# Kernel optimization log

Measured on AMD Instinct MI355X. Metric: run time of the kernel, lower is better.

## Reference

```python
import jax, jax.numpy as jnp
import numpy as np

B, T, D_IN, D_OUT = 4, 2048, 1024, 1024

def setup_inputs() -> dict:
    key = jax.random.key(0)
    k1, k2, k3, k4 = jax.random.split(key, 4)
    return {
        "vector": jax.random.normal(k1, (B, T, D_IN), dtype=jnp.float32),
        "W_queries": jax.random.normal(k2, (D_IN, D_OUT), dtype=jnp.float32),
        "W_keys": jax.random.normal(k3, (D_IN, D_OUT), dtype=jnp.float32),
        "W_values": jax.random.normal(k4, (D_IN, D_OUT), dtype=jnp.float32),
    }

def reference(vector, W_queries, W_keys, W_values):
    # vector: [B,T,d_in]; projections -> [B,T,d_out]
    q = vector @ W_queries
    k = vector @ W_keys
    v = vector @ W_values
    d_out = k.shape[-1]
    scores = jnp.einsum('btd,bsd->bts', q, k)  # [B,T,T]
    t = scores.shape[1]
    causal = jnp.tril(jnp.ones((t, t), dtype=bool))  # True = keep (mask is triu diag=1)
    scores = jnp.where(causal, scores, -jnp.inf)
    weights = jax.nn.softmax(scores / jnp.sqrt(jnp.float32(d_out)), axis=-1)
    # dropout p=0.0 -> identity
    return jnp.einsum('bts,bsd->btd', weights, v)
```

## Files before the change

### kernel.cpp

```cpp
#include <hip/hip_runtime.h>

#define TT   2048
#define DD   1024
#define BK   32

typedef float  f32x4  __attribute__((ext_vector_type(4)));
typedef __bf16 bf16x8 __attribute__((ext_vector_type(8)));

static __device__ __forceinline__ unsigned short f2bf(float f){
  unsigned int u = __float_as_uint(f);
  return (unsigned short)((u + 0x7fffu + ((u >> 16) & 1u)) >> 16);
}
static __device__ __forceinline__ float bf2f(unsigned short h){
  return __uint_as_float(((unsigned int)h) << 16);
}
static __device__ __forceinline__ bf16x8 ld8(const unsigned short* p){
  return *(const bf16x8*)p;
}
static __device__ __forceinline__ f32x4 mfma16(bf16x8 a, bf16x8 b, f32x4 c){
  return __builtin_amdgcn_mfma_f32_16x16x32_bf16(a, b, c, 0, 0, 0);
}

static __device__ __forceinline__ void async16(
    const unsigned short* g, unsigned short* l)
{
  __builtin_amdgcn_global_load_lds(
      (const __attribute__((address_space(1))) unsigned int*)g,
      (__attribute__((address_space(3))) unsigned int*)l, 16, 0, 0);
}

static __device__ __forceinline__ void stage_async(
    const unsigned short* __restrict__ src, int row_stride,
    unsigned short* __restrict__ dst, int t)
{
#pragma unroll
  for (int j = 0; j < 2; j++){
    int e = (t + j * 256) * 8;
    int row = e >> 5, col = e & 31;
    async16(src + (size_t)row * row_stride + col, dst + e);
  }
}

__global__ __launch_bounds__(256) void split_all_kernel(
    const float* __restrict__ X,  const float* __restrict__ Wq,
    const float* __restrict__ Wk, const float* __restrict__ Wv,
    unsigned short* __restrict__ Xhi,  unsigned short* __restrict__ Xlo,
    unsigned short* __restrict__ Wqhi, unsigned short* __restrict__ Wqlo,
    unsigned short* __restrict__ Wkhi, unsigned short* __restrict__ Wklo,
    unsigned short* __restrict__ WvThi)
{
  __shared__ float tile[32][33];
  int bx = blockIdx.x;
  if (bx < 10240){
    const float* src; unsigned short *hi, *lo; size_t base;
    if (bx < 8192)      { src = X;  hi = Xhi;  lo = Xlo;  base = (size_t)bx * 1024; }
    else if (bx < 9216) { src = Wq; hi = Wqhi; lo = Wqlo; base = (size_t)(bx - 8192) * 1024; }
    else                { src = Wk; hi = Wkhi; lo = Wklo; base = (size_t)(bx - 9216) * 1024; }
    size_t i = base + (size_t)threadIdx.x * 4;
    const float4 x = *(const float4*)(src + i);
    ushort4 h, l;
    h.x = f2bf(x.x); l.x = f2bf(x.x - bf2f(h.x));
    h.y = f2bf(x.y); l.y = f2bf(x.y - bf2f(h.y));
    h.z = f2bf(x.z); l.z = f2bf(x.z - bf2f(h.z));
    h.w = f2bf(x.w); l.w = f2bf(x.w - bf2f(h.w));
    *(ushort4*)(hi + i) = h;
    *(ushort4*)(lo + i) = l;
  } else {
    int tid = bx - 10240;
    int k0 = (tid & 31) * 32, n0 = (tid >> 5) * 32;
    int tx = threadIdx.x & 31, ty = threadIdx.x >> 5;
#pragma unroll
    for (int r = 0; r < 4; r++){
      int row = ty + r * 8;
      tile[row][tx] = Wv[(size_t)(k0 + row) * DD + n0 + tx];
    }
    __syncthreads();
#pragma unroll
    for (int r = 0; r < 4; r++){
      int nrow = ty + r * 8;
      float v = tile[tx][nrow];
      WvThi[(size_t)(n0 + nrow) * DD + k0 + tx] = f2bf(v);
    }
  }
}

__global__ __launch_bounds__(256) void mt_kernel(
    const unsigned short* __restrict__ Wkhi, const unsigned short* __restrict__ Wklo,
    const unsigned short* __restrict__ Wqhi, const unsigned short* __restrict__ Wqlo,
    unsigned short* __restrict__ MThi, unsigned short* __restrict__ MTlo)
{
  __shared__ unsigned short Ahi[128 * BK], Alo[128 * BK];
  __shared__ unsigned short Bhi[128 * BK], Blo[128 * BK];
  int e0 = blockIdx.y * 128, d0 = blockIdx.x * 128;
  const unsigned short* Ah_g = Wkhi + (size_t)e0 * DD;
  const unsigned short* Al_g = Wklo + (size_t)e0 * DD;
  const unsigned short* Bh_g = Wqhi + (size_t)d0 * DD;
  const unsigned short* Bl_g = Wqlo + (size_t)d0 * DD;
  int t = threadIdx.x;
  int lane = t & 63, w = t >> 6;
  int mw = (w >> 1) << 6, nw = (w & 1) << 6;
  int frow = lane & 15, fk = (lane >> 4) << 3;

  f32x4 acc[4][4];
#pragma unroll
  for (int a = 0; a < 4; a++)
#pragma unroll
    for (int c = 0; c < 4; c++){ f32x4 zz = {0.f,0.f,0.f,0.f}; acc[a][c] = zz; }

  for (int kk = 0; kk < DD / BK; kk++){
    int k0 = kk * BK;
    stage_async(Ah_g + k0, DD, Ahi, t);
    stage_async(Al_g + k0, DD, Alo, t);
    stage_async(Bh_g + k0, DD, Bhi, t);
    stage_async(Bl_g + k0, DD, Blo, t);
    __syncthreads();

    bf16x8 ah[4], al[4], bh[4], bl[4];
#pragma unroll
    for (int tm = 0; tm < 4; tm++){
      int off = (mw + tm * 16 + frow) * BK + fk;
      ah[tm] = ld8(&Ahi[off]); al[tm] = ld8(&Alo[off]);
    }
#pragma unroll
    for (int tn = 0; tn < 4; tn++){
      int off = (nw + tn * 16 + frow) * BK + fk;
      bh[tn] = ld8(&Bhi[off]); bl[tn] = ld8(&Blo[off]);
    }
#pragma unroll
    for (int tm = 0; tm < 4; tm++)
#pragma unroll
      for (int tn = 0; tn < 4; tn++){
        acc[tm][tn] = mfma16(ah[tm], bh[tn], acc[tm][tn]);
        acc[tm][tn] = mfma16(ah[tm], bl[tn], acc[tm][tn]);
        acc[tm][tn] = mfma16(al[tm], bh[tn], acc[tm][tn]);
      }
    __syncthreads();
  }

#pragma unroll
  for (int tm = 0; tm < 4; tm++)
#pragma unroll
    for (int tn = 0; tn < 4; tn++)
#pragma unroll
      for (int r = 0; r < 4; r++){
        float v = acc[tm][tn][r];
        int ge = e0 + mw + tm * 16 + ((lane >> 4) << 2) + r;
        int gd = d0 + nw + tn * 16 + frow;
        size_t idx = (size_t)ge * DD + gd;
        unsigned short h = f2bf(v);
        MThi[idx] = h; MTlo[idx] = f2bf(v - bf2f(h));
      }
}

__global__ __launch_bounds__(256, 2) void y_kernel(
    const unsigned short* __restrict__ Xhi, const unsigned short* __restrict__ Xlo,
    const unsigned short* __restrict__ MThi, const unsigned short* __restrict__ MTlo,
    const unsigned short* __restrict__ WvThi,
    unsigned short* __restrict__ Yhi, unsigned short* __restrict__ Ylo,
    unsigned short* __restrict__ VT)
{
  __shared__ unsigned short Ahs[128 * BK], Als[128 * BK];
  __shared__ unsigned short Bmh[128 * BK], Bml[128 * BK], Bvh[128 * BK];
  int m0 = blockIdx.x * 128, n0 = blockIdx.y * 128;
  const unsigned short* Ah_g  = Xhi   + (size_t)m0 * DD;
  const unsigned short* Al_g  = Xlo   + (size_t)m0 * DD;
  const unsigned short* Bmh_g = MThi  + (size_t)n0 * DD;
  const unsigned short* Bml_g = MTlo  + (size_t)n0 * DD;
  const unsigned short* Bvh_g = WvThi + (size_t)n0 * DD;
  int t = threadIdx.x;
  int lane = t & 63, w = t >> 6;
  int mw = (w >> 1) << 6, nw = (w & 1) << 6;
  int frow = lane & 15, fk = (lane >> 4) << 3;

  f32x4 accY[4][4], accV[4][4];
#pragma unroll
  for (int a = 0; a < 4; a++)
#pragma unroll
    for (int c = 0; c < 4; c++){
      f32x4 zz = {0.f,0.f,0.f,0.f}; accY[a][c] = zz; accV[a][c] = zz;
    }

  for (int kk = 0; kk < DD / BK; kk++){
    int k0 = kk * BK;
    stage_async(Ah_g  + k0, DD, Ahs, t);
    stage_async(Al_g  + k0, DD, Als, t);
    stage_async(Bmh_g + k0, DD, Bmh, t);
    stage_async(Bml_g + k0, DD, Bml, t);
    stage_async(Bvh_g + k0, DD, Bvh, t);
    __syncthreads();

    bf16x8 ah[4], al[4];
#pragma unroll
    for (int tm = 0; tm < 4; tm++){
      int off = (mw + tm * 16 + frow) * BK + fk;
      ah[tm] = ld8(&Ahs[off]); al[tm] = ld8(&Als[off]);
    }
#pragma unroll
    for (int tn = 0; tn < 4; tn++){
      int off = (nw + tn * 16 + frow) * BK + fk;
      bf16x8 bmh = ld8(&Bmh[off]), bml = ld8(&Bml[off]), bvh = ld8(&Bvh[off]);
#pragma unroll
      for (int tm = 0; tm < 4; tm++){
        accY[tm][tn] = mfma16(ah[tm], bmh, accY[tm][tn]);
        accY[tm][tn] = mfma16(ah[tm], bml, accY[tm][tn]);
        accY[tm][tn] = mfma16(al[tm], bmh, accY[tm][tn]);
        accV[tm][tn] = mfma16(ah[tm], bvh, accV[tm][tn]);
      }
    }
    __syncthreads();
  }

#pragma unroll
  for (int tm = 0; tm < 4; tm++)
#pragma unroll
    for (int tn = 0; tn < 4; tn++)
#pragma unroll
      for (int r = 0; r < 4; r++){
        int grow = m0 + mw + tm * 16 + ((lane >> 4) << 2) + r;
        int gcol = n0 + nw + tn * 16 + frow;
        size_t idx = (size_t)grow * DD + gcol;
        float vy = accY[tm][tn][r];
        unsigned short hy = f2bf(vy);
        Yhi[idx] = hy; Ylo[idx] = f2bf(vy - bf2f(hy));
        int b = grow >> 11, tl = grow & 2047;
        VT[((size_t)(b * DD + gcol) << 11) | tl] = f2bf(accV[tm][tn][r]);
      }
}

__global__ __launch_bounds__(256) void s_kernel(
    const unsigned short* __restrict__ Yhi, const unsigned short* __restrict__ Ylo,
    const unsigned short* __restrict__ Xhi, const unsigned short* __restrict__ Xlo,
    float* __restrict__ S)
{
  __shared__ unsigned short Ahi[128 * BK], Alo[128 * BK];
  __shared__ unsigned short Bhi[128 * BK], Blo[128 * BK];
  int bx = blockIdx.x;
  int nt = (bx < 32) ? 2 : 1;
  int u0 = (bx < 32) ? (480 + bx) : (bx - 32);
  int t = threadIdx.x;
  int lane = t & 63, w = t >> 6;
  int mw = (w >> 1) << 6, nw = (w & 1) << 6;
  int frow = lane & 15, fk = (lane >> 4) << 3;

  for (int sub = 0; sub < nt; sub++){
    int u = u0 + sub * 32;
    int b = u & 3;
    int tid = u >> 2;
    int bi = (int)((sqrtf(8.f * (float)tid + 1.f) - 1.f) * 0.5f);
    while ((bi + 1) * (bi + 2) / 2 <= tid) bi++;
    while (bi * (bi + 1) / 2 > tid) bi--;
    int bj = tid - bi * (bi + 1) / 2;
    int i0 = bi * 128, j0 = bj * 128;
    const unsigned short* Ah_g = Yhi + (size_t)(b * TT + i0) * DD;
    const unsigned short* Al_g = Ylo + (size_t)(b * TT + i0) * DD;
    const unsigned short* Bh_g = Xhi + (size_t)(b * TT + j0) * DD;
    const unsigned short* Bl_g = Xlo + (size_t)(b * TT + j0) * DD;

    f32x4 acc[4][4];
#pragma unroll
    for (int a = 0; a < 4; a++)
#pragma unroll
      for (int c = 0; c < 4; c++){ f32x4 zz = {0.f,0.f,0.f,0.f}; acc[a][c] = zz; }

    for (int kk = 0; kk < DD / BK; kk++){
      int k0 = kk * BK;
      stage_async(Ah_g + k0, DD, Ahi, t);
      stage_async(Al_g + k0, DD, Alo, t);
      stage_async(Bh_g + k0, DD, Bhi, t);
      stage_async(Bl_g + k0, DD, Blo, t);
      __syncthreads();

      bf16x8 ah[4], al[4], bh[4], bl[4];
#pragma unroll
      for (int tm = 0; tm < 4; tm++){
        int off = (mw + tm * 16 + frow) * BK + fk;
        ah[tm] = ld8(&Ahi[off]); al[tm] = ld8(&Alo[off]);
      }
#pragma unroll
      for (int tn = 0; tn < 4; tn++){
        int off = (nw + tn * 16 + frow) * BK + fk;
        bh[tn] = ld8(&Bhi[off]); bl[tn] = ld8(&Blo[off]);
      }
#pragma unroll
      for (int tm = 0; tm < 4; tm++)
#pragma unroll
        for (int tn = 0; tn < 4; tn++){
          acc[tm][tn] = mfma16(ah[tm], bh[tn], acc[tm][tn]);
          acc[tm][tn] = mfma16(ah[tm], bl[tn], acc[tm][tn]);
          acc[tm][tn] = mfma16(al[tm], bh[tn], acc[tm][tn]);
        }
      __syncthreads();
    }

#pragma unroll
    for (int tm = 0; tm < 4; tm++)
#pragma unroll
      for (int tn = 0; tn < 4; tn++)
#pragma unroll
        for (int r = 0; r < 4; r++){
          int gi = i0 + mw + tm * 16 + ((lane >> 4) << 2) + r;
          int gj = j0 + nw + tn * 16 + frow;
          S[((size_t)(b * TT + gi) * TT) + gj] = acc[tm][tn][r] * 0.03125f;
        }
  }
}

__global__ __launch_bounds__(256) void softmax_kernel(
    const float* __restrict__ S, unsigned short* __restrict__ P)
{
  int i = blockIdx.x, b = blockIdx.y;
  const float* s = S + (size_t)(b * TT + i) * TT;
  unsigned short* p = P + (size_t)(b * TT + i) * TT;
  int n = i + 1;
  int npad = ((i >> 7) + 1) << 7;
  int t = threadIdx.x;
  __shared__ float red[256];

  float v[8];
  float mx = -1e30f;
#pragma unroll
  for (int pas = 0; pas < 2; pas++){
    int idx = t * 4 + pas * 1024;
    if (idx + 3 < n){
      float4 x = *(const float4*)(s + idx);
      v[pas*4+0] = x.x; v[pas*4+1] = x.y; v[pas*4+2] = x.z; v[pas*4+3] = x.w;
    } else {
#pragma unroll
      for (int e = 0; e < 4; e++)
        v[pas*4+e] = (idx + e < n) ? s[idx + e] : -1e30f;
    }
#pragma unroll
    for (int e = 0; e < 4; e++) mx = fmaxf(mx, v[pas*4+e]);
  }
  red[t] = mx; __syncthreads();
  for (int k = 128; k > 0; k >>= 1){ if (t < k) red[t] = fmaxf(red[t], red[t + k]); __syncthreads(); }
  mx = red[0]; __syncthreads();

  float sum = 0.f;
#pragma unroll
  for (int j = 0; j < 8; j++){
    v[j] = __expf(v[j] - mx);
    sum += v[j];
  }
  red[t] = sum; __syncthreads();
  for (int k = 128; k > 0; k >>= 1){ if (t < k) red[t] += red[t + k]; __syncthreads(); }
  float inv = 1.0f / red[0];

#pragma unroll
  for (int pas = 0; pas < 2; pas++){
    int idx = t * 4 + pas * 1024;
    if (idx < npad){
      ushort4 o;
      o.x = f2bf(v[pas*4+0] * inv);
      o.y = f2bf(v[pas*4+1] * inv);
      o.z = f2bf(v[pas*4+2] * inv);
      o.w = f2bf(v[pas*4+3] * inv);
      *(ushort4*)(p + idx) = o;
    }
  }
}

__global__ __launch_bounds__(256) void pv_kernel(
    const unsigned short* __restrict__ P, const unsigned short* __restrict__ VT,
    float* __restrict__ O)
{
  __shared__ unsigned short At[128 * BK];
  __shared__ unsigned short Bt[128 * BK];
  int b  = blockIdx.z;
  int by = (int)gridDim.y - 1 - blockIdx.y;
  int i0 = by * 128, n0 = blockIdx.x * 128;
  int ksteps = (by + 1) * 4;
  const unsigned short* A_g = P  + (size_t)(b * TT + i0) * TT;
  const unsigned short* B_g = VT + (size_t)(b * DD + n0) * TT;
  int t = threadIdx.x;
  int lane = t & 63, w = t >> 6;
  int mw = (w >> 1) << 6, nw = (w & 1) << 6;
  int frow = lane & 15, fk = (lane >> 4) << 3;

  f32x4 acc[4][4];
#pragma unroll
  for (int a = 0; a < 4; a++)
#pragma unroll
    for (int c = 0; c < 4; c++){ f32x4 zz = {0.f,0.f,0.f,0.f}; acc[a][c] = zz; }

  for (int kk = 0; kk < ksteps; kk++){
    int k0 = kk * BK;
    stage_async(A_g + k0, TT, At, t);
    stage_async(B_g + k0, TT, Bt, t);
    __syncthreads();

    bf16x8 af[4], bf[4];
#pragma unroll
    for (int tm = 0; tm < 4; tm++) af[tm] = ld8(&At[(mw + tm * 16 + frow) * BK + fk]);
#pragma unroll
    for (int tn = 0; tn < 4; tn++) bf[tn] = ld8(&Bt[(nw + tn * 16 + frow) * BK + fk]);
#pragma unroll
    for (int tm = 0; tm < 4; tm++)
#pragma unroll
      for (int tn = 0; tn < 4; tn++)
        acc[tm][tn] = mfma16(af[tm], bf[tn], acc[tm][tn]);
    __syncthreads();
  }

#pragma unroll
  for (int tm = 0; tm < 4; tm++)
#pragma unroll
    for (int tn = 0; tn < 4; tn++)
#pragma unroll
      for (int r = 0; r < 4; r++){
        int gi = i0 + mw + tm * 16 + ((lane >> 4) << 2) + r;
        int gd = n0 + nw + tn * 16 + frow;
        O[(size_t)(b * TT + gi) * DD + gd] = acc[tm][tn][r];
      }
}

extern "C" void kernel_launch(void* const* d_in, const int* in_sizes, int n_in,
                              void* d_out, int out_size, void* d_ws, size_t ws_size,
                              hipStream_t stream) {
  const float* X  = (const float*)d_in[0];
  const float* Wq = (const float*)d_in[1];
  const float* Wk = (const float*)d_in[2];
  const float* Wv = (const float*)d_in[3];
  float* Out = (float*)d_out;

  const size_t M1 = 1048576u;
  unsigned short* base  = (unsigned short*)d_ws;
  unsigned short* Wqhi  = base;
  unsigned short* Wqlo  = base + 1 * M1;
  unsigned short* Wkhi  = base + 2 * M1;
  unsigned short* Wklo  = base + 3 * M1;
  unsigned short* WvThi = base + 4 * M1;
  unsigned short* MThi  = base + 5 * M1;
  unsigned short* MTlo  = base + 6 * M1;
  unsigned short* Xhi   = base + 7 * M1;
  unsigned short* Xlo   = base + 15 * M1;
  unsigned short* Yhi   = base + 23 * M1;
  unsigned short* Ylo   = base + 31 * M1;
  unsigned short* VT    = base + 39 * M1;
  float*          S     = (float*)(base + 47 * M1);
  unsigned short* P     = Xhi;

  dim3 blk(256);
  split_all_kernel<<<dim3(11264), blk, 0, stream>>>(X, Wq, Wk, Wv,
      Xhi, Xlo, Wqhi, Wqlo, Wkhi, Wklo, WvThi);
  mt_kernel<<<dim3(8, 8), blk, 0, stream>>>(Wkhi, Wklo, Wqhi, Wqlo, MThi, MTlo);
  y_kernel<<<dim3(64, 8), blk, 0, stream>>>(Xhi, Xlo, MThi, MTlo, WvThi, Yhi, Ylo, VT);
  s_kernel<<<dim3(512), blk, 0, stream>>>(Yhi, Ylo, Xhi, Xlo, S);
  softmax_kernel<<<dim3(2048, 4, 1), blk, 0, stream>>>(S, P);
  pv_kernel<<<dim3(8, 16, 4), blk, 0, stream>>>(P, VT, Out);
}
```

Before: 360.3 us.

## Split-K the last 32 score tiles and reduce partials inside softmax

The old score kernel ran 512 blocks, with 32 blocks doing two tiles each to cover 544 lower-triangle tiles. Now 512 blocks each do one full tile, and the last 32 tiles are split four ways along K into 128 extra blocks. The first K-quarter writes to S and the other three write partial sums to a separate buffer, which softmax adds back for rows 1920 and up. This evens out the per-block work and removes the two-tile tail, at the cost of extra partial-sum traffic and an unconditional float4 load in softmax that can read past the causal range.

```diff
diff --git a/kernel.cpp b/kernel.cpp
--- a/kernel.cpp
+++ b/kernel.cpp
@@ -230,68 +230,72 @@
 __global__ __launch_bounds__(256) void s_kernel(
     const unsigned short* __restrict__ Yhi, const unsigned short* __restrict__ Ylo,
     const unsigned short* __restrict__ Xhi, const unsigned short* __restrict__ Xlo,
-    float* __restrict__ S)
+    float* __restrict__ S, float* __restrict__ Spart)
 {
   __shared__ unsigned short Ahi[128 * BK], Alo[128 * BK];
   __shared__ unsigned short Bhi[128 * BK], Blo[128 * BK];
   int bx = blockIdx.x;
-  int nt = (bx < 32) ? 2 : 1;
-  int u0 = (bx < 32) ? (480 + bx) : (bx - 32);
+  int u, q, kbeg, kend;
+  if (bx < 512){ u = bx; q = 0; kbeg = 0; kend = 32; }
+  else {
+    int e = bx - 512;
+    q = e & 3;
+    u = 512 + (e >> 2);
+    kbeg = q * 8; kend = kbeg + 8;
+  }
+  int b = u & 3;
+  int tid = u >> 2;
+  int bi = (int)((sqrtf(8.f * (float)tid + 1.f) - 1.f) * 0.5f);
+  while ((bi + 1) * (bi + 2) / 2 <= tid) bi++;
+  while (bi * (bi + 1) / 2 > tid) bi--;
+  int bj = tid - bi * (bi + 1) / 2;
+  int i0 = bi * 128, j0 = bj * 128;
+  const unsigned short* Ah_g = Yhi + (size_t)(b * TT + i0) * DD;
+  const unsigned short* Al_g = Ylo + (size_t)(b * TT + i0) * DD;
+  const unsigned short* Bh_g = Xhi + (size_t)(b * TT + j0) * DD;
+  const unsigned short* Bl_g = Xlo + (size_t)(b * TT + j0) * DD;
   int t = threadIdx.x;
   int lane = t & 63, w = t >> 6;
   int mw = (w >> 1) << 6, nw = (w & 1) << 6;
   int frow = lane & 15, fk = (lane >> 4) << 3;
 
-  for (int sub = 0; sub < nt; sub++){
-    int u = u0 + sub * 32;
-    int b = u & 3;
-    int tid = u >> 2;
-    int bi = (int)((sqrtf(8.f * (float)tid + 1.f) - 1.f) * 0.5f);
-    while ((bi + 1) * (bi + 2) / 2 <= tid) bi++;
-    while (bi * (bi + 1) / 2 > tid) bi--;
-    int bj = tid - bi * (bi + 1) / 2;
-    int i0 = bi * 128, j0 = bj * 128;
-    const unsigned short* Ah_g = Yhi + (size_t)(b * TT + i0) * DD;
-    const unsigned short* Al_g = Ylo + (size_t)(b * TT + i0) * DD;
-    const unsigned short* Bh_g = Xhi + (size_t)(b * TT + j0) * DD;
-    const unsigned short* Bl_g = Xlo + (size_t)(b * TT + j0) * DD;
-
-    f32x4 acc[4][4];
-#pragma unroll
-    for (int a = 0; a < 4; a++)
-#pragma unroll
-      for (int c = 0; c < 4; c++){ f32x4 zz = {0.f,0.f,0.f,0.f}; acc[a][c] = zz; }
-
-    for (int kk = 0; kk < DD / BK; kk++){
-      int k0 = kk * BK;
-      stage_async(Ah_g + k0, DD, Ahi, t);
-      stage_async(Al_g + k0, DD, Alo, t);
-      stage_async(Bh_g + k0, DD, Bhi, t);
-      stage_async(Bl_g + k0, DD, Blo, t);
-      __syncthreads();
-
-      bf16x8 ah[4], al[4], bh[4], bl[4];
-#pragma unroll
-      for (int tm = 0; tm < 4; tm++){
-        int off = (mw + tm * 16 + frow) * BK + fk;
-        ah[tm] = ld8(&Ahi[off]); al[tm] = ld8(&Alo[off]);
-      }
+  f32x4 acc[4][4];
+#pragma unroll
+  for (int a = 0; a < 4; a++)
+#pragma unroll
+    for (int c = 0; c < 4; c++){ f32x4 zz = {0.f,0.f,0.f,0.f}; acc[a][c] = zz; }
+
+  for (int kk = kbeg; kk < kend; kk++){
+    int k0 = kk * BK;
+    stage_async(Ah_g + k0, DD, Ahi, t);
+    stage_async(Al_g + k0, DD, Alo, t);
+    stage_async(Bh_g + k0, DD, Bhi, t);
+    stage_async(Bl_g + k0, DD, Blo, t);
+    __syncthreads();
+
+    bf16x8 ah[4], al[4], bh[4], bl[4];
+#pragma unroll
+    for (int tm = 0; tm < 4; tm++){
+      int off = (mw + tm * 16 + frow) * BK + fk;
+      ah[tm] = ld8(&Ahi[off]); al[tm] = ld8(&Alo[off]);
+    }
+#pragma unroll
+    for (int tn = 0; tn < 4; tn++){
+      int off = (nw + tn * 16 + frow) * BK + fk;
+      bh[tn] = ld8(&Bhi[off]); bl[tn] = ld8(&Blo[off]);
+    }
+#pragma unroll
+    for (int tm = 0; tm < 4; tm++)
 #pragma unroll
       for (int tn = 0; tn < 4; tn++){
-        int off = (nw + tn * 16 + frow) * BK + fk;
-        bh[tn] = ld8(&Bhi[off]); bl[tn] = ld8(&Blo[off]);
-      }
-#pragma unroll
-      for (int tm = 0; tm < 4; tm++)
-#pragma unroll
-        for (int tn = 0; tn < 4; tn++){
-          acc[tm][tn] = mfma16(ah[tm], bh[tn], acc[tm][tn]);
-          acc[tm][tn] = mfma16(ah[tm], bl[tn], acc[tm][tn]);
-          acc[tm][tn] = mfma16(al[tm], bh[tn], acc[tm][tn]);
-        }
-      __syncthreads();
-    }
-
+        acc[tm][tn] = mfma16(ah[tm], bh[tn], acc[tm][tn]);
+        acc[tm][tn] = mfma16(ah[tm], bl[tn], acc[tm][tn]);
+        acc[tm][tn] = mfma16(al[tm], bh[tn], acc[tm][tn]);
+      }
+    __syncthreads();
+  }
+
+  if (q == 0){
 #pragma unroll
     for (int tm = 0; tm < 4; tm++)
 #pragma unroll
@@ -302,11 +306,24 @@
           int gj = j0 + nw + tn * 16 + frow;
           S[((size_t)(b * TT + gi) * TT) + gj] = acc[tm][tn][r] * 0.03125f;
         }
+  } else {
+    float* dst = Spart + ((size_t)(q - 1) * 32 + (u - 512)) * 16384;
+#pragma unroll
+    for (int tm = 0; tm < 4; tm++)
+#pragma unroll
+      for (int tn = 0; tn < 4; tn++)
+#pragma unroll
+        for (int r = 0; r < 4; r++){
+          int row = mw + tm * 16 + ((lane >> 4) << 2) + r;
+          int col = nw + tn * 16 + frow;
+          dst[row * 128 + col] = acc[tm][tn][r] * 0.03125f;
+        }
   }
 }
 
 __global__ __launch_bounds__(256) void softmax_kernel(
-    const float* __restrict__ S, unsigned short* __restrict__ P)
+    const float* __restrict__ S, const float* __restrict__ Spart,
+    unsigned short* __restrict__ P)
 {
   int i = blockIdx.x, b = blockIdx.y;
   const float* s = S + (size_t)(b * TT + i) * TT;
@@ -314,6 +331,7 @@
   int n = i + 1;
   int npad = ((i >> 7) + 1) << 7;
   int t = threadIdx.x;
+  bool qrow = (i >= 1920);
   __shared__ float red[256];
 
   float v[8];
@@ -321,14 +339,23 @@
 #pragma unroll
   for (int pas = 0; pas < 2; pas++){
     int idx = t * 4 + pas * 1024;
-    if (idx + 3 < n){
-      float4 x = *(const float4*)(s + idx);
-      v[pas*4+0] = x.x; v[pas*4+1] = x.y; v[pas*4+2] = x.z; v[pas*4+3] = x.w;
-    } else {
-#pragma unroll
-      for (int e = 0; e < 4; e++)
-        v[pas*4+e] = (idx + e < n) ? s[idx + e] : -1e30f;
-    }
+    float4 x = *(const float4*)(s + idx);
+    if (qrow && pas == 1){
+      int jt = (idx - 1024) >> 7;
+      int qt = 4 * jt + b;
+      size_t base = (size_t)qt * 16384 + (size_t)(i - 1920) * 128 + ((idx - 1024) & 127);
+      const float4 p1 = *(const float4*)(Spart + base);
+      const float4 p2 = *(const float4*)(Spart + 32 * 16384 + base);
+      const float4 p3 = *(const float4*)(Spart + 2 * 32 * 16384 + base);
+      x.x += p1.x + p2.x + p3.x;
+      x.y += p1.y + p2.y + p3.y;
+      x.z += p1.z + p2.z + p3.z;
+      x.w += p1.w + p2.w + p3.w;
+    }
+    v[pas*4+0] = (idx + 0 < n) ? x.x : -1e30f;
+    v[pas*4+1] = (idx + 1 < n) ? x.y : -1e30f;
+    v[pas*4+2] = (idx + 2 < n) ? x.z : -1e30f;
+    v[pas*4+3] = (idx + 3 < n) ? x.w : -1e30f;
 #pragma unroll
     for (int e = 0; e < 4; e++) mx = fmaxf(mx, v[pas*4+e]);
   }
@@ -438,6 +465,7 @@
   unsigned short* Ylo   = base + 31 * M1;
   unsigned short* VT    = base + 39 * M1;
   float*          S     = (float*)(base + 47 * M1);
+  float*          Spart = (float*)(base + 79 * M1);
   unsigned short* P     = Xhi;
 
   dim3 blk(256);
@@ -445,7 +473,7 @@
       Xhi, Xlo, Wqhi, Wqlo, Wkhi, Wklo, WvThi);
   mt_kernel<<<dim3(8, 8), blk, 0, stream>>>(Wkhi, Wklo, Wqhi, Wqlo, MThi, MTlo);
   y_kernel<<<dim3(64, 8), blk, 0, stream>>>(Xhi, Xlo, MThi, MTlo, WvThi, Yhi, Ylo, VT);
-  s_kernel<<<dim3(512), blk, 0, stream>>>(Yhi, Ylo, Xhi, Xlo, S);
-  softmax_kernel<<<dim3(2048, 4, 1), blk, 0, stream>>>(S, P);
+  s_kernel<<<dim3(640), blk, 0, stream>>>(Yhi, Ylo, Xhi, Xlo, S, Spart);
+  softmax_kernel<<<dim3(2048, 4, 1), blk, 0, stream>>>(S, Spart, P);
   pv_kernel<<<dim3(8, 16, 4), blk, 0, stream>>>(P, VT, Out);
 }
```

Measured after the change: 340.8 us. -5.4%, faster.
